# Performance work log

Measured on AMD Instinct MI355X. Metric: run time of the kernel, lower is better.

Reference implementation:

```python
import jax, jax.numpy as jnp
from jax import lax
import numpy as np

B, N = 64, 8192


def setup_inputs() -> dict:
    key = jax.random.key(0)
    ks = jax.random.split(key, 8)
    v = jax.random.normal(ks[0], (B, N), jnp.float32)
    mask = (jax.random.uniform(ks[1], (B, N)) > 0.5).astype(jnp.float32)
    def init_w(k, shape, fan_in):
        return (jax.random.normal(k, shape, jnp.float32) / np.float32(np.sqrt(fan_in)))
    # Conv1d weights: (out_ch, in_ch, kernel)
    w1 = init_w(ks[2], (32, 2, 5), 2 * 5)
    b1 = jnp.zeros((32,), jnp.float32)
    w2 = init_w(ks[3], (32, 32, 5), 32 * 5)
    b2 = jnp.zeros((32,), jnp.float32)
    w3 = init_w(ks[4], (2, 32, 5), 32 * 5)
    b3 = jnp.zeros((2,), jnp.float32)
    return dict(v=v, mask=mask, w1=w1, b1=b1, w2=w2, b2=b2, w3=w3, b3=b3)


def _bk_gii(he_diag):
    """Diagonal of G = (zI - H)^{-1} for tridiagonal H (diag=he_diag, sub=super=1), z=1j.
    Uses the standard left/right continued-fraction recursions:
      L_0 = z - a_0,   L_i = z - a_i - 1/L_{i-1}
      R_{N-1} = z - a_{N-1},   R_i = z - a_i - 1/R_{i+1}
      G_ii = 1 / (L_i + R_i - (z - a_i))
    Returns (B, N, 2) features = [Re G_ii, Im G_ii]."""
    z = jnp.complex64(1j)
    a = he_diag.astype(jnp.complex64).T  # (N, B)

    def step(carry, a_i):
        nxt = z - a_i - 1.0 / carry
        return nxt, nxt

    L0 = z - a[0]
    _, Ls = lax.scan(step, L0, a[1:])
    L = jnp.concatenate([L0[None], Ls], axis=0)  # (N, B)

    Rl = z - a[-1]
    _, Rs = lax.scan(step, Rl, a[:-1][::-1])
    R = jnp.concatenate([Rl[None], Rs], axis=0)[::-1]  # (N, B)

    G = 1.0 / (L + R - (z - a))  # (N, B) complex
    return jnp.stack([G.real, G.imag], axis=-1).transpose(1, 0, 2)  # (B, N, 2)


def _conv1d(x, w, b):
    # x: (B, C_in, N), w: (C_out, C_in, K=5), 'same' padding (pad=2)
    y = lax.conv_general_dilated(x, w, window_strides=(1,), padding=[(2, 2)],
                                 dimension_numbers=('NCH', 'OIH', 'NCH'))
    return y + b[None, :, None]


def reference(v, mask, w1, b1, w2, b2, w3, b3):
    he_diag = v - 2.0  # h0_diag_base (-2.0) + v
    feats_full = _bk_gii(he_diag)                 # (B, N, 2)
    feats_sparse = feats_full * mask[..., None]   # zero out unmasked positions
    # learned interpolator: Conv1d(2->32)->ReLU->Conv1d(32->32)->ReLU->Conv1d(32->2)
    x = feats_sparse.transpose(0, 2, 1)           # (B, 2, N)
    x = jax.nn.relu(_conv1d(x, w1, b1))
    x = jax.nn.relu(_conv1d(x, w2, b2))
    feats_interp = _conv1d(x, w3, b3).transpose(0, 2, 1)  # (B, N, 2)
    feats_final = jnp.where(mask[..., None] > 0.5, feats_sparse, feats_interp)
    return feats_final, feats_sparse
```

## Files before the change

kernel.cpp:

```cpp
#include <hip/hip_runtime.h>
#include <hip/hip_bf16.h>


#define BB 64
#define NN 8192
#define KWARM 16
#define TSEG 1024
#define H 8
#define PCH 8
#define NCH 130
#define STG0 320
#define CHK 256
#define NT 512
#define HST 40

using half8  = __attribute__((ext_vector_type(8))) _Float16;
using f32x16 = __attribute__((ext_vector_type(16))) float;

#define FENCE() asm volatile("" ::: "memory")

__device__ __forceinline__ half8 ld16(const ushort* p) {
    return *reinterpret_cast<const half8*>(p);
}
__device__ __forceinline__ ushort f2h(float x) {
    _Float16 h = (_Float16)x;
    return __builtin_bit_cast(unsigned short, h);
}
__device__ __forceinline__ uint pk2rn(float a, float b) {
    union { _Float16 h[2]; uint u; } r;
    r.h[0] = (_Float16)a; r.h[1] = (_Float16)b;
    return r.u;
}
__device__ __forceinline__ float h2f(ushort u) {
    return (float)__builtin_bit_cast(_Float16, u);
}

#define CSTV(RV, IV, AV) { float dd_ = RV*RV + IV*IV;                      \
    float iv_ = __builtin_amdgcn_rcpf(dd_);                                \
    float nr_ = -(AV) - RV*iv_;                                            \
    IV = 1.0f + IV*iv_; RV = nr_; }
#define GC(LRV, LIV, RRV, RIV, AV, MM, GR, GI) {                           \
    float Dr_ = LRV + RRV + (AV), Di_ = LIV + RIV - 1.0f;                  \
    float iv_ = __builtin_amdgcn_rcpf(Dr_*Dr_ + Di_*Di_);                  \
    GR = Dr_*iv_*(MM); GI = -Di_*iv_*(MM); }

__global__ __launch_bounds__(NT, 4) void fused_kernel(
    const float* __restrict__ v,  const float* __restrict__ mask,
    const float* __restrict__ w1, const float* __restrict__ b1,
    const float* __restrict__ w2, const float* __restrict__ b2,
    const float* __restrict__ w3, const float* __restrict__ b3,
    float* __restrict__ outF, float* __restrict__ fs)
{
    __shared__ __align__(16) ushort h1t[264 * HST];
    __shared__ __align__(16) ushort h2t[260 * HST];
    __shared__ __align__(16) ushort wt1c[32 * 32];
    __shared__ __align__(16) ushort wt2c[32 * 176];
    __shared__ __align__(16) ushort wt3c[2 * 160];
    __shared__ __align__(16) uint   xsp[TSEG + 2*H + 8];
    __shared__ __align__(8) unsigned char mskb[TSEG];
    __shared__ float b3s[2];

    const int tid  = threadIdx.x;
    const int b    = blockIdx.y;
    const int s    = blockIdx.x * TSEG;
    const int base = s - H - KWARM;

    float* sa = reinterpret_cast<float*>(h1t);

    for (int i = tid; i < TSEG + 2*H + 2*KWARM; i += NT) {
        int g = base + i; g = min(max(g, 0), NN - 1);
        sa[i] = v[b * NN + g] - 2.0f;
    }
    __syncthreads();

    if (tid < NCH) {
        const int e0 = s - H + PCH * tid;
        if (e0 >= 0 && e0 + PCH <= NN) {
            float4 mva = *reinterpret_cast<const float4*>(&mask[b * NN + e0]);
            float4 mvb = *reinterpret_cast<const float4*>(&mask[b * NN + e0 + 4]);
            const float4* s4 = reinterpret_cast<const float4*>(sa);
            float4 aA = s4[2*tid + 4];
            float4 aB = s4[2*tid + 5];
            float Lr, Li, Rr, Ri;
            const bool fast = (e0 - KWARM >= 0) && (e0 + 7 + KWARM <= NN - 1);
            if (fast) {
                float4 cL = s4[2*tid];
                float4 cR = s4[2*tid + 9];
                Lr = -cL.x; Li = 1.0f; Rr = -cR.w; Ri = 1.0f;
                CSTV(Lr, Li, cL.y); CSTV(Rr, Ri, cR.z);
                CSTV(Lr, Li, cL.z); CSTV(Rr, Ri, cR.y);
                CSTV(Lr, Li, cL.w); CSTV(Rr, Ri, cR.x);
                #pragma unroll
                for (int g = 1; g <= 3; ++g) {
                    float4 nL = s4[2*tid + g];
                    float4 nR = s4[2*tid + 9 - g];
                    CSTV(Lr, Li, nL.x); CSTV(Rr, Ri, nR.w);
                    CSTV(Lr, Li, nL.y); CSTV(Rr, Ri, nR.z);
                    CSTV(Lr, Li, nL.z); CSTV(Rr, Ri, nR.y);
                    CSTV(Lr, Li, nL.w); CSTV(Rr, Ri, nR.x);
                }
                CSTV(Lr, Li, aA.x);
                CSTV(Rr, Ri, aB.w);
            } else {
                int j0 = max(e0 - KWARM, 0);
                Lr = -sa[j0 - base]; Li = 1.0f;
                for (int j = j0 + 1; j <= e0; ++j) CSTV(Lr, Li, sa[j - base]);
                int j1 = min(e0 + 7 + KWARM, NN - 1);
                Rr = -sa[j1 - base]; Ri = 1.0f;
                for (int j = j1 - 1; j >= e0 + 7; --j) CSTV(Rr, Ri, sa[j - base]);
            }
            float L0r = Lr, L0i = Li;
            CSTV(Lr, Li, aA.y); float L1r = Lr, L1i = Li;
            CSTV(Lr, Li, aA.z); float L2r = Lr, L2i = Li;
            CSTV(Lr, Li, aA.w); float L3r = Lr, L3i = Li;
            CSTV(Lr, Li, aB.x); float L4r = Lr, L4i = Li;
            CSTV(Lr, Li, aB.y); float L5r = Lr, L5i = Li;
            CSTV(Lr, Li, aB.z); float L6r = Lr, L6i = Li;
            CSTV(Lr, Li, aB.w); float L7r = Lr, L7i = Li;
            float g0r,g0i,g1r,g1i,g2r,g2i,g3r,g3i,g4r,g4i,g5r,g5i,g6r,g6i,g7r,g7i;
            GC(L7r, L7i, Rr, Ri, aB.w, mvb.w, g7r, g7i);
            CSTV(Rr, Ri, aB.z); GC(L6r, L6i, Rr, Ri, aB.z, mvb.z, g6r, g6i);
            CSTV(Rr, Ri, aB.y); GC(L5r, L5i, Rr, Ri, aB.y, mvb.y, g5r, g5i);
            CSTV(Rr, Ri, aB.x); GC(L4r, L4i, Rr, Ri, aB.x, mvb.x, g4r, g4i);
            CSTV(Rr, Ri, aA.w); GC(L3r, L3i, Rr, Ri, aA.w, mva.w, g3r, g3i);
            CSTV(Rr, Ri, aA.z); GC(L2r, L2i, Rr, Ri, aA.z, mva.z, g2r, g2i);
            CSTV(Rr, Ri, aA.y); GC(L1r, L1i, Rr, Ri, aA.y, mva.y, g1r, g1i);
            CSTV(Rr, Ri, aA.x); GC(L0r, L0i, Rr, Ri, aA.x, mva.x, g0r, g0i);

            uint4 pkA, pkB;
            pkA.x = (uint)f2h(g0r) | ((uint)f2h(g0i) << 16);
            pkA.y = (uint)f2h(g1r) | ((uint)f2h(g1i) << 16);
            pkA.z = (uint)f2h(g2r) | ((uint)f2h(g2i) << 16);
            pkA.w = (uint)f2h(g3r) | ((uint)f2h(g3i) << 16);
            pkB.x = (uint)f2h(g4r) | ((uint)f2h(g4i) << 16);
            pkB.y = (uint)f2h(g5r) | ((uint)f2h(g5i) << 16);
            pkB.z = (uint)f2h(g6r) | ((uint)f2h(g6i) << 16);
            pkB.w = (uint)f2h(g7r) | ((uint)f2h(g7i) << 16);
            *reinterpret_cast<uint4*>(&xsp[PCH * tid])     = pkA;
            *reinterpret_cast<uint4*>(&xsp[PCH * tid + 4]) = pkB;

            if (e0 >= s && e0 < s + TSEG) {
                size_t off = ((size_t)b * NN + e0) * 2;
                *reinterpret_cast<float4*>(&fs[off])      = make_float4(g0r, g0i, g1r, g1i);
                *reinterpret_cast<float4*>(&fs[off + 4])  = make_float4(g2r, g2i, g3r, g3i);
                *reinterpret_cast<float4*>(&fs[off + 8])  = make_float4(g4r, g4i, g5r, g5i);
                *reinterpret_cast<float4*>(&fs[off + 12]) = make_float4(g6r, g6i, g7r, g7i);
                uint mb0 = (mva.x > 0.5f ? 1u : 0u) | (mva.y > 0.5f ? 1u : 0u) << 8
                         | (mva.z > 0.5f ? 1u : 0u) << 16 | (mva.w > 0.5f ? 1u : 0u) << 24;
                uint mb1 = (mvb.x > 0.5f ? 1u : 0u) | (mvb.y > 0.5f ? 1u : 0u) << 8
                         | (mvb.z > 0.5f ? 1u : 0u) << 16 | (mvb.w > 0.5f ? 1u : 0u) << 24;
                *reinterpret_cast<uint2*>(&mskb[e0 - s]) = make_uint2(mb0, mb1);
            }
        } else {
            uint4 z = {0u, 0u, 0u, 0u};
            *reinterpret_cast<uint4*>(&xsp[PCH * tid])     = z;
            *reinterpret_cast<uint4*>(&xsp[PCH * tid + 4]) = z;
        }
    } else if (tid < NCH + 8) {
        xsp[TSEG + 2*H + (tid - NCH)] = 0u;
    } else if (tid >= STG0) {
        const int t0 = tid - STG0;
        for (int i = t0; i < 1024; i += 192) {
            int co = i >> 5, k = i & 31;
            ushort val = 0;
            if (k < 10)       val = f2h(w1[co*10 + (k&1)*5 + (k>>1)]);
            else if (k == 10) val = f2h(b1[co]);
            wt1c[i] = val;
        }
        for (int i = t0; i < 5120; i += 192) {
            int co = i / 160, r = i - co*160;
            wt2c[co*176 + (r % 5)*32 + r/5] = f2h(w2[i]);
        }
        for (int i = t0; i < 512; i += 192) {
            int co = i >> 4, k = 160 + (i & 15);
            wt2c[co*176 + k] = (k == 160) ? f2h(b2[co]) : (ushort)0;
        }
        for (int i = t0; i < 320; i += 192) {
            int co = i / 160, r = i - co*160;
            wt3c[co*160 + (r % 5)*32 + r/5] = f2h(w3[i]);
        }
        if (t0 < 2) b3s[t0] = b3[t0];
    }
    __syncthreads();

    const int lane = tid & 63;
    const int wv   = tid >> 6;
    const int cn   = lane & 31;
    const int kh   = lane >> 5;
    const int kh4  = 4 * kh;

    union { half8 v8; uint u[4]; } on;
    on.u[0] = kh ? 0u : 0x3C00u; on.u[1] = 0u; on.u[2] = 0u; on.u[3] = 0u;
    const half8 onesF = on.v8;

    half8 wA1 = ld16(&wt1c[cn * 32 + 8 * kh]);
    half8 wA2[11];
    #pragma unroll
    for (int t = 0; t < 11; ++t) wA2[t] = ld16(&wt2c[cn*176 + 16*t + 8*kh]);
    const float bz0 = b3s[0], bz1 = b3s[1];

    auto conv1_tile = [&](int cr, int tb1) {
        int mi = cr + 2 + tb1 + cn;
        union { half8 v8; uint u[4]; } B;
        if (kh == 0) { B.u[0]=xsp[mi];   B.u[1]=xsp[mi+1];
                       B.u[2]=xsp[mi+2]; B.u[3]=xsp[mi+3]; }
        else         { B.u[0]=xsp[mi+4]; B.u[1]=0x3C00u;
                       B.u[2]=0; B.u[3]=0; }
        f32x16 a1 = {};
        a1 = __builtin_amdgcn_mfma_f32_32x32x16_f16(wA1, B.v8, a1, 0, 0, 0);
        int row = tb1 + cn;
        int gp  = s + cr - 4 + row;
        bool ok = (gp >= 0) && (gp < NN);
        ushort* rp = &h1t[row * HST + kh4];
        #pragma unroll
        for (int q = 0; q < 4; ++q) {
            uint lo = pk2rn(fmaxf(a1[4*q+0], 0.f), fmaxf(a1[4*q+1], 0.f));
            uint hi = pk2rn(fmaxf(a1[4*q+2], 0.f), fmaxf(a1[4*q+3], 0.f));
            *reinterpret_cast<uint2*>(rp + 8*q) =
                make_uint2(ok ? lo : 0u, ok ? hi : 0u);
        }
    };
    auto conv2_tile = [&](int cr, int tb2) {
        f32x16 acc = {};
        #pragma unroll
        for (int q = 0; q < 10; ++q) {
            int kidx = 16*q + 8*kh;
            half8 Bf = ld16(&h1t[(tb2 + cn + (kidx >> 5))*HST + (kidx & 31)]);
            acc = __builtin_amdgcn_mfma_f32_32x32x16_f16(wA2[q], Bf, acc, 0, 0, 0);
        }
        acc = __builtin_amdgcn_mfma_f32_32x32x16_f16(wA2[10], onesF, acc, 0, 0, 0);
        int row = tb2 + cn;
        int gp  = s + cr - 2 + row;
        bool ok = (gp >= 0) && (gp < NN);
        ushort* rp = &h2t[row * HST + kh4];
        #pragma unroll
        for (int q = 0; q < 4; ++q) {
            uint lo = pk2rn(fmaxf(acc[4*q+0], 0.f), fmaxf(acc[4*q+1], 0.f));
            uint hi = pk2rn(fmaxf(acc[4*q+2], 0.f), fmaxf(acc[4*q+3], 0.f));
            *reinterpret_cast<uint2*>(rp + 8*q) =
                make_uint2(ok ? lo : 0u, ok ? hi : 0u);
        }
    };

    for (int ch = 0; ch < 4; ++ch) {
        const int cr = ch * CHK;

        if (ch == 0) {
            conv1_tile(cr, 32 * wv);
            if (wv == 0) conv1_tile(cr, 232);
        } else {
            conv1_tile(cr, 8 + 32 * wv);
        }
        __syncthreads();

        if (ch == 0) {
            conv2_tile(cr, 32 * wv);
            if (wv == 1) conv2_tile(cr, 228);
        } else {
            conv2_tile(cr, 4 + 32 * wv);
        }
        if (ch < 3 && wv == 0 && lane < 40) {
            FENCE();
            int r = lane / 10, q = lane % 10;
            *reinterpret_cast<uint2*>(&h1t[(4 + r)*HST + 4*q]) =
                *reinterpret_cast<const uint2*>(&h1t[(260 + r)*HST + 4*q]);
        }
        __syncthreads();

        {
            const int tb3 = 32 * wv;
            f32x16 a3 = {};
            half8 z = {};
            const int wb = ((cn < 2) ? cn : 0) * 160;
            #pragma unroll
            for (int q = 0; q < 10; ++q) {
                int kidx = 16*q + 8*kh;
                half8 Af = (cn < 2) ? ld16(&wt3c[wb + 16*q + 8*kh]) : z;
                half8 Bf = ld16(&h2t[(tb3 + cn + (kidx >> 5))*HST + (kidx & 31)]);
                a3 = __builtin_amdgcn_mfma_f32_32x32x16_f16(Af, Bf, a3, 0, 0, 0);
            }
            if (kh == 0) {
                int p = cr + tb3 + cn;
                uint xp = xsp[H + p];
                bool m  = mskb[p] != 0;
                float ox = m ? h2f((ushort)(xp & 0xffffu)) : (a3[0] + bz0);
                float oy = m ? h2f((ushort)(xp >> 16))     : (a3[1] + bz1);
                *reinterpret_cast<float2*>(&outF[((size_t)b*NN + s + p)*2]) =
                    make_float2(ox, oy);
            }
        }
        if (ch < 3 && wv == 0 && lane < 40) {
            FENCE();
            int r = lane / 10, q = lane % 10;
            *reinterpret_cast<uint2*>(&h2t[r*HST + 4*q]) =
                *reinterpret_cast<const uint2*>(&h2t[(256 + r)*HST + 4*q]);
        }
    }
}

extern "C" void kernel_launch(void* const* d_in, const int* in_sizes, int n_in,
                              void* d_out, int out_size, void* d_ws, size_t ws_size,
                              hipStream_t stream) {
    const float* v    = (const float*)d_in[0];
    const float* mask = (const float*)d_in[1];
    const float* w1   = (const float*)d_in[2];
    const float* b1   = (const float*)d_in[3];
    const float* w2   = (const float*)d_in[4];
    const float* b2   = (const float*)d_in[5];
    const float* w3   = (const float*)d_in[6];
    const float* b3   = (const float*)d_in[7];

    float* outF = (float*)d_out;
    float* fs   = outF + (size_t)BB * NN * 2;

    dim3 g(NN / TSEG, BB);
    fused_kernel<<<g, NT, 0, stream>>>(v, mask, w1, b1, w2, b2, w3, b3, outF, fs);
}
```

Baseline: 23.99 us.

## Halve block to 256 threads with each wave computing two conv tiles

Cuts the block from 8 waves to 4, so each wave now processes two 32-row tiles per conv stage, interleaving their MFMA chains and sharing the weight fragments. Weight-staging threads are re-partitioned to fit the smaller block. The aim is more ILP per wave and less barrier cost, while accepting fewer waves per block and a halved launch-bounds occupancy hint. The serial tridiagonal recursion phase now has fewer spare threads to overlap the weight staging with.

```diff
diff --git a/kernel.cpp b/kernel.cpp
--- a/kernel.cpp
+++ b/kernel.cpp
@@ -9,9 +9,10 @@
 #define H 8
 #define PCH 8
 #define NCH 130
-#define STG0 320
+#define STG0 138
+#define NSTG 118
 #define CHK 256
-#define NT 512
+#define NT 256
 #define HST 40
 
 using half8  = __attribute__((ext_vector_type(8))) _Float16;
@@ -44,7 +45,7 @@
     float iv_ = __builtin_amdgcn_rcpf(Dr_*Dr_ + Di_*Di_);                  \
     GR = Dr_*iv_*(MM); GI = -Di_*iv_*(MM); }
 
-__global__ __launch_bounds__(NT, 4) void fused_kernel(
+__global__ __launch_bounds__(NT, 2) void fused_kernel(
     const float* __restrict__ v,  const float* __restrict__ mask,
     const float* __restrict__ w1, const float* __restrict__ b1,
     const float* __restrict__ w2, const float* __restrict__ b2,
@@ -156,26 +157,26 @@
             *reinterpret_cast<uint4*>(&xsp[PCH * tid])     = z;
             *reinterpret_cast<uint4*>(&xsp[PCH * tid + 4]) = z;
         }
-    } else if (tid < NCH + 8) {
+    } else if (tid < STG0) {
         xsp[TSEG + 2*H + (tid - NCH)] = 0u;
-    } else if (tid >= STG0) {
+    } else {
         const int t0 = tid - STG0;
-        for (int i = t0; i < 1024; i += 192) {
+        for (int i = t0; i < 1024; i += NSTG) {
             int co = i >> 5, k = i & 31;
             ushort val = 0;
             if (k < 10)       val = f2h(w1[co*10 + (k&1)*5 + (k>>1)]);
             else if (k == 10) val = f2h(b1[co]);
             wt1c[i] = val;
         }
-        for (int i = t0; i < 5120; i += 192) {
+        for (int i = t0; i < 5120; i += NSTG) {
             int co = i / 160, r = i - co*160;
             wt2c[co*176 + (r % 5)*32 + r/5] = f2h(w2[i]);
         }
-        for (int i = t0; i < 512; i += 192) {
+        for (int i = t0; i < 512; i += NSTG) {
             int co = i >> 4, k = 160 + (i & 15);
             wt2c[co*176 + k] = (k == 160) ? f2h(b2[co]) : (ushort)0;
         }
-        for (int i = t0; i < 320; i += 192) {
+        for (int i = t0; i < 320; i += NSTG) {
             int co = i / 160, r = i - co*160;
             wt3c[co*160 + (r % 5)*32 + r/5] = f2h(w3[i]);
         }
@@ -220,25 +221,33 @@
                 make_uint2(ok ? lo : 0u, ok ? hi : 0u);
         }
     };
-    auto conv2_tile = [&](int cr, int tb2) {
-        f32x16 acc = {};
+    auto conv2_pair = [&](int cr, int tbA, int tbB) {
+        f32x16 accA = {}, accB = {};
         #pragma unroll
         for (int q = 0; q < 10; ++q) {
             int kidx = 16*q + 8*kh;
-            half8 Bf = ld16(&h1t[(tb2 + cn + (kidx >> 5))*HST + (kidx & 31)]);
-            acc = __builtin_amdgcn_mfma_f32_32x32x16_f16(wA2[q], Bf, acc, 0, 0, 0);
-        }
-        acc = __builtin_amdgcn_mfma_f32_32x32x16_f16(wA2[10], onesF, acc, 0, 0, 0);
-        int row = tb2 + cn;
-        int gp  = s + cr - 2 + row;
-        bool ok = (gp >= 0) && (gp < NN);
-        ushort* rp = &h2t[row * HST + kh4];
+            int ro = (kidx >> 5), co2 = (kidx & 31);
+            half8 BfA = ld16(&h1t[(tbA + cn + ro)*HST + co2]);
+            half8 BfB = ld16(&h1t[(tbB + cn + ro)*HST + co2]);
+            accA = __builtin_amdgcn_mfma_f32_32x32x16_f16(wA2[q], BfA, accA, 0, 0, 0);
+            accB = __builtin_amdgcn_mfma_f32_32x32x16_f16(wA2[q], BfB, accB, 0, 0, 0);
+        }
+        accA = __builtin_amdgcn_mfma_f32_32x32x16_f16(wA2[10], onesF, accA, 0, 0, 0);
+        accB = __builtin_amdgcn_mfma_f32_32x32x16_f16(wA2[10], onesF, accB, 0, 0, 0);
         #pragma unroll
-        for (int q = 0; q < 4; ++q) {
-            uint lo = pk2rn(fmaxf(acc[4*q+0], 0.f), fmaxf(acc[4*q+1], 0.f));
-            uint hi = pk2rn(fmaxf(acc[4*q+2], 0.f), fmaxf(acc[4*q+3], 0.f));
-            *reinterpret_cast<uint2*>(rp + 8*q) =
-                make_uint2(ok ? lo : 0u, ok ? hi : 0u);
+        for (int t2 = 0; t2 < 2; ++t2) {
+            const f32x16& acc = t2 ? accB : accA;
+            int row = (t2 ? tbB : tbA) + cn;
+            int gp  = s + cr - 2 + row;
+            bool ok = (gp >= 0) && (gp < NN);
+            ushort* rp = &h2t[row * HST + kh4];
+            #pragma unroll
+            for (int q = 0; q < 4; ++q) {
+                uint lo = pk2rn(fmaxf(acc[4*q+0], 0.f), fmaxf(acc[4*q+1], 0.f));
+                uint hi = pk2rn(fmaxf(acc[4*q+2], 0.f), fmaxf(acc[4*q+3], 0.f));
+                *reinterpret_cast<uint2*>(rp + 8*q) =
+                    make_uint2(ok ? lo : 0u, ok ? hi : 0u);
+            }
         }
     };
 
@@ -247,17 +256,19 @@
 
         if (ch == 0) {
             conv1_tile(cr, 32 * wv);
+            conv1_tile(cr, 32 * (wv + 4));
             if (wv == 0) conv1_tile(cr, 232);
         } else {
             conv1_tile(cr, 8 + 32 * wv);
+            conv1_tile(cr, 8 + 32 * (wv + 4));
         }
         __syncthreads();
 
         if (ch == 0) {
-            conv2_tile(cr, 32 * wv);
-            if (wv == 1) conv2_tile(cr, 228);
+            conv2_pair(cr, 32 * wv, 32 * (wv + 4));
+            if (wv == 1) conv2_pair(cr, 228, 228);
         } else {
-            conv2_tile(cr, 4 + 32 * wv);
+            conv2_pair(cr, 4 + 32 * wv, 4 + 32 * (wv + 4));
         }
         if (ch < 3 && wv == 0 && lane < 40) {
             FENCE();
@@ -268,25 +279,32 @@
         __syncthreads();
 
         {
-            const int tb3 = 32 * wv;
-            f32x16 a3 = {};
+            const int tbA = 32 * wv, tbB = 32 * (wv + 4);
+            f32x16 aA = {}, aB = {};
             half8 z = {};
             const int wb = ((cn < 2) ? cn : 0) * 160;
             #pragma unroll
             for (int q = 0; q < 10; ++q) {
                 int kidx = 16*q + 8*kh;
-                half8 Af = (cn < 2) ? ld16(&wt3c[wb + 16*q + 8*kh]) : z;
-                half8 Bf = ld16(&h2t[(tb3 + cn + (kidx >> 5))*HST + (kidx & 31)]);
-                a3 = __builtin_amdgcn_mfma_f32_32x32x16_f16(Af, Bf, a3, 0, 0, 0);
+                int ro = (kidx >> 5), co2 = (kidx & 31);
+                half8 Af  = (cn < 2) ? ld16(&wt3c[wb + 16*q + 8*kh]) : z;
+                half8 BfA = ld16(&h2t[(tbA + cn + ro)*HST + co2]);
+                half8 BfB = ld16(&h2t[(tbB + cn + ro)*HST + co2]);
+                aA = __builtin_amdgcn_mfma_f32_32x32x16_f16(Af, BfA, aA, 0, 0, 0);
+                aB = __builtin_amdgcn_mfma_f32_32x32x16_f16(Af, BfB, aB, 0, 0, 0);
             }
             if (kh == 0) {
-                int p = cr + tb3 + cn;
-                uint xp = xsp[H + p];
-                bool m  = mskb[p] != 0;
-                float ox = m ? h2f((ushort)(xp & 0xffffu)) : (a3[0] + bz0);
-                float oy = m ? h2f((ushort)(xp >> 16))     : (a3[1] + bz1);
-                *reinterpret_cast<float2*>(&outF[((size_t)b*NN + s + p)*2]) =
-                    make_float2(ox, oy);
+                #pragma unroll
+                for (int t3 = 0; t3 < 2; ++t3) {
+                    const f32x16& a3 = t3 ? aB : aA;
+                    int p = cr + (t3 ? tbB : tbA) + cn;
+                    uint xp = xsp[H + p];
+                    bool m  = mskb[p] != 0;
+                    float ox = m ? h2f((ushort)(xp & 0xffffu)) : (a3[0] + bz0);
+                    float oy = m ? h2f((ushort)(xp >> 16))     : (a3[1] + bz1);
+                    *reinterpret_cast<float2*>(&outF[((size_t)b*NN + s + p)*2]) =
+                        make_float2(ox, oy);
+                }
             }
         }
         if (ch < 3 && wv == 0 && lane < 40) {
```

Measured after the change: 27.98 us. 1.17x slower.
